# Performance work log

Hardware: AMD Instinct MI355X
Metric: run time of the kernel (lower is better)

The kernel has to match this reference:

```python
import jax, jax.numpy as jnp
import numpy as np

# --- configuration (mirrors VFNet cfg) ---
B, NC = 1, 6                     # batch, surround cameras
C_IN, H_F, W_F = 64, 44, 80      # fused feature level (height//8, width//8)
XD, YD, ZD = 100, 100, 20        # voxel dims (x forward, inverse-depth spaced)
X0, X1 = 2.0, 51.5
Y0, Y1 = -25.0, 24.5
Z0, Z1 = -3.0, 2.7
DB, D_STR, D_END = 50, 2.0, 50.0 # projection depth bins (inverse-depth spaced)
VDIM, FOUT = 64, 256             # voxel_pre_dim, feat_out_dim
P = H_F * W_F
EPS = 1e-8


def _axes():
    ego_x = 1.0 / jnp.linspace(1.0 / X1, 1.0 / X0, XD)[::-1]  # ascending, nonuniform
    ego_y = jnp.linspace(Y0, Y1, YD)
    ego_z = jnp.linspace(Z0, Z1, ZD)
    return ego_x, ego_y, ego_z


def _voxel_pts():
    ex, ey, ez = _axes()
    gz, gy, gx = jnp.meshgrid(ez, ey, ex, indexing='ij')      # [Z,Y,X]
    pts = jnp.stack([gx, gy, gz], 0).reshape(3, -1)
    return jnp.concatenate([pts, jnp.ones((1, pts.shape[1]), pts.dtype)], 0)  # [4,N]


def _bilinear2d(img, u, v):
    C, H, W = img.shape
    u0, v0 = jnp.floor(u), jnp.floor(v)
    du, dv = u - u0, v - v0
    u0i = jnp.clip(u0.astype(jnp.int32), 0, W - 1); u1i = jnp.clip(u0i + 1, 0, W - 1)
    v0i = jnp.clip(v0.astype(jnp.int32), 0, H - 1); v1i = jnp.clip(v0i + 1, 0, H - 1)
    g = lambda vi, ui: img[:, vi, ui]
    return (g(v0i, u0i) * (1 - du) * (1 - dv) + g(v0i, u1i) * du * (1 - dv)
            + g(v1i, u0i) * (1 - du) * dv + g(v1i, u1i) * du * dv)


def _nonuniform_index(axis, q):
    # searchsorted + in-bin lerp: metric coord -> continuous index on nonuniform axis
    qc = jnp.clip(q, axis[0], axis[-1] - 1e-6)
    k = jnp.clip(jnp.searchsorted(axis, qc, side='left') - 1, 0, axis.shape[0] - 2)
    t = (qc - axis[k]) / (axis[k + 1] - axis[k] + 1e-12)
    return k.astype(qc.dtype) + t


def _trilinear(vol, xi, yi, zi):
    Cc, Zz, Yy, Xx = vol.shape
    def sp(i, n):
        i0 = jnp.floor(i); t = i - i0
        a = jnp.clip(i0.astype(jnp.int32), 0, n - 1)
        return a, jnp.clip(a + 1, 0, n - 1), t
    x0, x1, tx = sp(xi, Xx); y0, y1, ty = sp(yi, Yy); z0, z1, tz = sp(zi, Zz)
    g = lambda z, y, x: vol[:, z, y, x]
    c0 = (g(z0, y0, x0) * (1 - tx) + g(z0, y0, x1) * tx) * (1 - ty) + (g(z0, y1, x0) * (1 - tx) + g(z0, y1, x1) * tx) * ty
    c1 = (g(z1, y0, x0) * (1 - tx) + g(z1, y0, x1) * tx) * (1 - ty) + (g(z1, y1, x0) * (1 - tx) + g(z1, y1, x1) * tx) * ty
    return c0 * (1 - tz) + c1 * tz


def _conv2d(x, w, b):
    y = jax.lax.conv_general_dilated(x, w, (1, 1), 'SAME', dimension_numbers=('NCHW', 'OIHW', 'NCHW'))
    return y + b[None, :, None, None]


def _conv3d(x, w, b):
    y = jax.lax.conv_general_dilated(x, w, (1, 1, 1), 'SAME', dimension_numbers=('NCDHW', 'OIDHW', 'NCDHW'))
    return y + b[None, :, None, None, None]


def _forward(feats, masks, K, ext, w_ov, b_ov, w_no, b_no, w_fu, b_fu, w_r1, b_r1, w_r2, b_r2):
    ex, ey, ez = _axes()
    vpts = _voxel_pts()                                        # [4,N]
    fm = jnp.concatenate([feats[0], masks[0]], axis=1)         # [NC, C+1, H, W]
    ext_inv = jnp.linalg.inv(ext)

    # --- backproject surround-view features into the nonuniform voxel grid ---
    def per_cam(img, Kc, Ei):
        pix = Kc @ (Ei @ vpts)
        z = pix[2]
        u = pix[0] / (z + EPS); v = pix[1] / (z + EPS)
        valid = (z > EPS) & (u >= 0) & (u <= W_F - 1) & (v >= 0) & (v <= H_F - 1)
        return _bilinear2d(img, u, v) * valid, valid.astype(img.dtype)

    s, valid = jax.vmap(per_cam)(fm, K, ext_inv)               # [NC,C+1,N], [NC,N]
    count = valid.sum(0)
    cat = jnp.concatenate([s[:3].sum(0), s[3:].sum(0)], axis=0)  # [2*(C+1),N]
    ov = jax.nn.elu(w_ov @ cat + b_ov[:, None]) * (count == 2)
    no = jax.nn.elu(w_no @ s.sum(0) + b_no[:, None]) * (count == 1)
    vf = (ov + no).reshape(VDIM, ZD, YD, XD)                   # [64,Z,Y,X]

    # --- nonuniform-x -> uniform-x remap (searchsorted + lerp) + conv3d fusion ---
    xi_axis = _nonuniform_index(ex, jnp.linspace(X0, X1, XD))
    ZI, YI, XI = jnp.meshgrid(jnp.arange(ZD, dtype=vf.dtype), jnp.arange(YD, dtype=vf.dtype), xi_axis, indexing='ij')
    vf_remap = _trilinear(vf, XI, YI, ZI)
    vol = jax.nn.elu(_conv3d(jnp.concatenate([vf, vf_remap], 0)[None], w_fu, b_fu))[0]  # [64,Z,Y,X]

    # --- project fused voxel features into each camera frustum over inv-depth bins ---
    uu, vv = jnp.meshgrid(jnp.arange(W_F), jnp.arange(H_F), indexing='xy')
    pix_grid = jnp.stack([uu.reshape(-1).astype(feats.dtype), vv.reshape(-1).astype(feats.dtype), jnp.ones((P,), feats.dtype)], 0)  # [3,P]
    dbins = 1.0 / jnp.linspace(1.0 / D_END, 1.0 / D_STR, DB)[::-1]  # ascending, inv-depth spaced
    K3inv = jnp.linalg.inv(K[:, :3, :3])

    def per_cam_proj(Ki, Ec):
        dirs = Ki @ pix_grid                                   # [3,P]
        pc = dirs[:, None, :] * dbins[None, :, None]           # [3,D,P]
        pc = jnp.concatenate([pc, jnp.ones((1, DB, P), pc.dtype)], 0)
        pw = (Ec @ pc.reshape(4, -1)).reshape(4, DB, P)        # ego-frame points
        wx, wy, wz = pw[0], pw[1], pw[2]
        xi = _nonuniform_index(ex, wx)
        yi = (wy - Y0) / (Y1 - Y0) * (YD - 1)
        zi = (wz - Z0) / (Z1 - Z0) * (ZD - 1)
        inb = (wx >= X0) & (wx <= X1) & (yi >= 0) & (yi <= YD - 1) & (zi >= 0) & (zi <= ZD - 1)
        samp = _trilinear(vol, xi, yi, zi) * inb               # [64,D,P]
        return samp.reshape(VDIM * DB, H_F, W_F)

    proj = jax.vmap(per_cam_proj)(K3inv, ext)                  # [NC, 64*D, H, W]
    h = jax.nn.elu(_conv2d(proj, w_r1, b_r1))
    return jax.nn.elu(_conv2d(h, w_r2, b_r2))                  # [NC, 256, H, W]


def setup_inputs() -> dict:
    key = jax.random.key(0)
    ks = jax.random.split(key, 8)
    feats = jax.random.normal(ks[0], (B, NC, C_IN, H_F, W_F), jnp.float32)
    masks = jnp.ones((B, NC, 1, H_F, W_F), jnp.float32)
    Kn = np.eye(4, dtype=np.float32)
    Kn[0, 0] = Kn[1, 1] = 40.0; Kn[0, 2] = 40.0; Kn[1, 2] = 22.0  # ~90deg hfov at 80px
    K = np.tile(Kn, (NC, 1, 1))
    ext = np.zeros((NC, 4, 4), dtype=np.float32)
    for i in range(NC):
        th = 2 * np.pi * i / NC
        c, s0 = np.cos(th), np.sin(th)
        R = np.array([[s0, 0, c], [-c, 0, s0], [0, -1, 0]], dtype=np.float32)  # cam(right,down,fwd)->ego
        ext[i, :3, :3] = R
        ext[i, :3, 3] = np.array([c, s0, 0.8], dtype=np.float32)
        ext[i, 3, 3] = 1.0
    w_ov = jax.random.normal(ks[1], (VDIM, 2 * (C_IN + 1)), jnp.float32) / np.sqrt(2 * (C_IN + 1)).astype(np.float32)
    w_no = jax.random.normal(ks[2], (VDIM, C_IN + 1), jnp.float32) / np.sqrt(C_IN + 1).astype(np.float32)
    w_fu = jax.random.normal(ks[3], (VDIM, 2 * VDIM, 3, 3, 3), jnp.float32) / np.sqrt(2 * VDIM * 27).astype(np.float32)
    w_r1 = jax.random.normal(ks[4], (FOUT, VDIM * DB, 3, 3), jnp.float32) / np.sqrt(VDIM * DB * 9).astype(np.float32)
    w_r2 = jax.random.normal(ks[5], (FOUT, FOUT, 3, 3), jnp.float32) / np.sqrt(FOUT * 9).astype(np.float32)
    z = lambda n: jnp.zeros((n,), jnp.float32)
    return {"feats": feats, "masks": masks, "K": jnp.asarray(K), "ext": jnp.asarray(ext),
            "w_ov": w_ov, "b_ov": z(VDIM), "w_no": w_no, "b_no": z(VDIM),
            "w_fu": w_fu, "b_fu": z(VDIM), "w_r1": w_r1, "b_r1": z(FOUT),
            "w_r2": w_r2, "b_r2": z(FOUT)}


def reference(feats, masks, K, ext, w_ov, b_ov, w_no, b_no, w_fu, b_fu, w_r1, b_r1, w_r2, b_r2):
    return _forward(feats, masks, K, ext, w_ov, b_ov, w_no, b_no, w_fu, b_fu, w_r1, b_r1, w_r2, b_r2)
```

## Files before the change

### kernel.cpp

```cpp
#include <hip/hip_runtime.h>
#include <math.h>

#define NCAM 6
#define CIN  64
#define HF   44
#define WF   80
#define PP   (HF*WF)
#define XD   100
#define YD   100
#define ZD   20
#define NVOX (XD*YD*ZD)
#define DBN  50
#define VDIM 64
#define FOUT 256
#define EPSF 1e-8f

typedef _Float16 f16x4 __attribute__((ext_vector_type(4)));
typedef _Float16 f16x8 __attribute__((ext_vector_type(8)));
typedef float    f32x4 __attribute__((ext_vector_type(4)));

#define OFF_KE    0
#define OFF_K3I   96
#define OFF_XI    160
#define OFF_DBIN  260
#define OFF_WOVT  320
#define OFF_WNOT  8640
#define B_VOL     51200UL
#define B_WT1     51200UL
#define B_H       14796800UL
#define B_VIN     25651200UL
#define B_PROJ    25651200UL
#define B_WT2     25651200UL
#define B_WT3     76851200UL

__device__ __forceinline__ float eluf(float x) { return x > 0.f ? x : expm1f(x); }

#define AX_A    (1.0f/51.5f)
#define AX_STEP ((0.5f - 1.0f/51.5f)/99.0f)

__device__ __forceinline__ void inv3x3(const float m[9], float o[9]) {
    float a00 = m[4]*m[8] - m[5]*m[7];
    float a10 = m[5]*m[6] - m[3]*m[8];
    float a20 = m[3]*m[7] - m[4]*m[6];
    float det = m[0]*a00 + m[1]*a10 + m[2]*a20;
    float id = 1.0f/det;
    o[0] = a00*id;
    o[1] = (m[2]*m[7] - m[1]*m[8])*id;
    o[2] = (m[1]*m[5] - m[2]*m[4])*id;
    o[3] = a10*id;
    o[4] = (m[0]*m[8] - m[2]*m[6])*id;
    o[5] = (m[2]*m[3] - m[0]*m[5])*id;
    o[6] = a20*id;
    o[7] = (m[1]*m[6] - m[0]*m[7])*id;
    o[8] = (m[0]*m[4] - m[1]*m[3])*id;
}

__global__ __launch_bounds__(256) void setup_kernel(const float* K, const float* ext,
                                                    const float* w_ov, const float* w_no,
                                                    float* ws) {
    int t = threadIdx.x;
    if (t < NCAM) {
        const float* E = ext + t*16;
        float R[9] = {E[0],E[1],E[2], E[4],E[5],E[6], E[8],E[9],E[10]};
        float Ri[9];
        inv3x3(R, Ri);
        float tx=E[3], ty=E[7], tz=E[11];
        float bx = -(Ri[0]*tx + Ri[1]*ty + Ri[2]*tz);
        float by = -(Ri[3]*tx + Ri[4]*ty + Ri[5]*tz);
        float bz = -(Ri[6]*tx + Ri[7]*ty + Ri[8]*tz);
        float Ei[16] = {Ri[0],Ri[1],Ri[2],bx, Ri[3],Ri[4],Ri[5],by, Ri[6],Ri[7],Ri[8],bz, 0,0,0,1};
        const float* Km = K + t*16;
        float* KE = ws + OFF_KE + t*16;
        for (int r=0;r<4;r++)
            for (int c=0;c<4;c++) {
                float s=0.f;
                for (int k=0;k<4;k++) s += Km[r*4+k]*Ei[k*4+c];
                KE[r*4+c]=s;
            }
        float Kr[9] = {Km[0],Km[1],Km[2], Km[4],Km[5],Km[6], Km[8],Km[9],Km[10]};
        float Ki[9];
        inv3x3(Kr, Ki);
        float* KI = ws + OFF_K3I + t*9;
        for (int i=0;i<9;i++) KI[i]=Ki[i];
    }
    if (t >= 64 && t < 64+XD) {
        int x = t-64;
        float ex0 = 1.0f/(AX_A + 99.0f*AX_STEP);
        float exN = 1.0f/AX_A;
        float q = 2.0f + (float)x * (49.5f/99.0f);
        float qc = fminf(fmaxf(q, ex0), exN - 1e-6f);
        float f = 99.0f - (1.0f/qc - AX_A)/AX_STEP;
        int k = min(max((int)floorf(f),0),98);
        float exk  = 1.0f/(AX_A + (float)(99-k)*AX_STEP);
        float exk1 = 1.0f/(AX_A + (float)(98-k)*AX_STEP);
        ws[OFF_XI + x] = (float)k + (qc - exk)/(exk1 - exk + 1e-12f);
    }
    if (t >= 192 && t < 192+DBN) {
        int d = t-192;
        float sa = 1.0f/50.0f;
        float ss = (0.5f - sa)/49.0f;
        ws[OFF_DBIN + d] = 1.0f/(sa + (float)(49-d)*ss);
    }
    for (int i = t; i < 130*64; i += 256) {
        int k = i >> 6, c = i & 63;
        ws[OFF_WOVT + i] = w_ov[c*130 + k];
    }
    for (int i = t; i < 65*64; i += 256) {
        int k = i >> 6, c = i & 63;
        ws[OFF_WNOT + i] = w_no[c*65 + k];
    }
}

__global__ __launch_bounds__(256) void tw1_kernel(const float* w, _Float16* o) {
    int idx = blockIdx.x*256 + threadIdx.x;
    int cp  = idx % 3200;
    int oc  = (idx/3200) & 255;
    int tap = idx/(3200*256);
    int d = cp >> 6, v = cp & 63;
    o[idx] = (_Float16)w[((size_t)oc*3200 + v*50 + d)*9 + tap];
}
__global__ __launch_bounds__(256) void tw2_kernel(const float* w, _Float16* o) {
    int idx = blockIdx.x*256 + threadIdx.x;
    int ic  = idx & 255;
    int oc  = (idx >> 8) & 255;
    int tap = idx >> 16;
    o[idx] = (_Float16)w[((size_t)oc*256 + ic)*9 + tap];
}
__global__ __launch_bounds__(256) void tw3_kernel(const float* w, _Float16* o) {
    int idx = blockIdx.x*256 + threadIdx.x;
    int ci  = idx & 127;
    int oc  = (idx >> 7) & 63;
    int tap = idx >> 13;
    o[idx] = (_Float16)w[((size_t)oc*128 + ci)*27 + tap];
}

__global__ __launch_bounds__(256) void backproject_kernel(const float* feats, const float* masks,
                                                          const float* ws,
                                                          const float* b_ov, const float* b_no,
                                                          _Float16* vin) {
    int wave = threadIdx.x >> 6;
    int lane = threadIdx.x & 63;
    int n = blockIdx.x*4 + wave;
    int x = n % XD;
    int y = (n / XD) % YD;
    int z = n / (XD*YD);
    float gx = 1.0f/(AX_A + (float)(99-x)*AX_STEP);
    float gy = -25.0f + (float)y * (49.5f/99.0f);
    float gz = -3.0f  + (float)z * (5.7f/19.0f);

    float sA = 0.f, sB = 0.f, sA64 = 0.f, sB64 = 0.f;
    int cnt = 0;
    for (int cam = 0; cam < NCAM; ++cam) {
        const float* KE = ws + OFF_KE + cam*16;
        float px = KE[0]*gx + KE[1]*gy + KE[2]*gz + KE[3];
        float py = KE[4]*gx + KE[5]*gy + KE[6]*gz + KE[7];
        float pz = KE[8]*gx + KE[9]*gy + KE[10]*gz + KE[11];
        float inv = 1.0f/(pz + EPSF);
        float u = px*inv, v = py*inv;
        bool valid = (pz > EPSF) && (u >= 0.f) && (u <= 79.f) && (v >= 0.f) && (v <= 43.f);
        if (valid) {
            cnt++;
            float u0 = floorf(u), v0 = floorf(v);
            float du = u-u0, dv = v-v0;
            int u0i = min(max((int)u0,0),WF-1), u1i = min(u0i+1,WF-1);
            int v0i = min(max((int)v0,0),HF-1), v1i = min(v0i+1,HF-1);
            float w00=(1.f-du)*(1.f-dv), w01=du*(1.f-dv), w10=(1.f-du)*dv, w11=du*dv;
            int i00=v0i*WF+u0i, i01=v0i*WF+u1i, i10=v1i*WF+u0i, i11=v1i*WF+u1i;
            const float* img = feats + (cam*CIN + lane)*PP;
            float val = w00*img[i00] + w01*img[i01] + w10*img[i10] + w11*img[i11];
            const float* mg = masks + cam*PP;
            float mv = w00*mg[i00] + w01*mg[i01] + w10*mg[i10] + w11*mg[i11];
            if (cam < 3) { sA += val; sA64 += mv; }
            else         { sB += val; sB64 += mv; }
        }
    }
    float out = 0.f;
    if (cnt == 2) {
        const float* wT = ws + OFF_WOVT;
        float acc = b_ov[lane];
        for (int k = 0; k < 64; ++k) {
            float ca = __shfl(sA, k, 64);
            float cb = __shfl(sB, k, 64);
            acc += wT[k*64 + lane]*ca + wT[(65+k)*64 + lane]*cb;
        }
        acc += wT[64*64 + lane]*sA64 + wT[129*64 + lane]*sB64;
        out = eluf(acc);
    } else if (cnt == 1) {
        const float* wT = ws + OFF_WNOT;
        float s = sA + sB, s64 = sA64 + sB64;
        float acc = b_no[lane];
        for (int k = 0; k < 64; ++k) {
            float ca = __shfl(s, k, 64);
            acc += wT[k*64 + lane]*ca;
        }
        acc += wT[64*64 + lane]*s64;
        out = eluf(acc);
    }
    vin[(size_t)n*128 + lane] = (_Float16)out;
}

__global__ __launch_bounds__(256) void remap_kernel(const float* ws, _Float16* vin) {
    int wave = threadIdx.x >> 6, lane = threadIdx.x & 63;
    int n = blockIdx.x*4 + wave;
    int x = n % XD;
    float xi = ws[OFF_XI + x];
    float fx = floorf(xi);
    float t = xi - fx;
    int x0 = min(max((int)fx,0),XD-1);
    int x1 = min(x0+1, XD-1);
    size_t rowb = (size_t)(n - x)*128;
    float r = (float)vin[rowb + (size_t)x0*128 + lane]*(1.f-t)
            + (float)vin[rowb + (size_t)x1*128 + lane]*t;
    vin[(size_t)n*128 + 64 + lane] = (_Float16)r;
}

__global__ __launch_bounds__(256,2) void conv3d_mfma_kernel(const _Float16* __restrict__ vin,
                                                            const _Float16* __restrict__ wT,
                                                            const float* __restrict__ bias,
                                                            _Float16* __restrict__ vol) {
    __shared__ __align__(16) _Float16 Bs[9*104*36];
    int tid = threadIdx.x, lane = tid & 63, wave = tid >> 6;
    int ln = lane & 15, kq = lane >> 4;
    int y = blockIdx.x % 100, z = blockIdx.x / 100;
    int nt0 = wave*2;
    int ntn = (wave == 3) ? 1 : 2;
    f32x4 zero4 = {0.f,0.f,0.f,0.f};
    f32x4 acc[4][2];
    for (int i=0;i<4;i++) for (int t=0;t<2;t++) acc[i][t] = zero4;

    for (int c0 = 0; c0 < 128; c0 += 32) {
        __syncthreads();
        for (int g = tid; g < 9*104*4; g += 256) {
            int ic8 = g & 3;
            int xe  = (g >> 2) % 104;
            int rid = g / (104*4);
            int xx = xe - 1, yy = y + rid%3 - 1, zz = z + rid/3 - 1;
            f16x8 val = {0,0,0,0,0,0,0,0};
            if (xx >= 0 && xx < 100 && yy >= 0 && yy < 100 && zz >= 0 && zz < 20)
                val = *(const f16x8*)(vin + (size_t)((zz*100 + yy)*100 + xx)*128 + c0 + ic8*8);
            *(f16x8*)(&Bs[(rid*104 + xe)*36 + ic8*8]) = val;
        }
        __syncthreads();
        const _Float16* wp0 = wT + c0 + kq*8;
        f16x8 a0n = *(const f16x8*)(wp0 + (ln+ 0)*128);
        f16x8 a1n = *(const f16x8*)(wp0 + (ln+16)*128);
        f16x8 a2n = *(const f16x8*)(wp0 + (ln+32)*128);
        f16x8 a3n = *(const f16x8*)(wp0 + (ln+48)*128);
        for (int tap = 0; tap < 27; ++tap) {
            f16x8 a0 = a0n, a1 = a1n, a2 = a2n, a3 = a3n;
            if (tap < 26) {
                const _Float16* wp = wT + (size_t)(tap+1)*64*128 + c0 + kq*8;
                a0n = *(const f16x8*)(wp + (ln+ 0)*128);
                a1n = *(const f16x8*)(wp + (ln+16)*128);
                a2n = *(const f16x8*)(wp + (ln+32)*128);
                a3n = *(const f16x8*)(wp + (ln+48)*128);
            }
            int dx = tap % 3, rid = tap / 3;
            for (int t = 0; t < ntn; ++t) {
                int xe = min(16*(nt0+t) + ln + dx, 103);
                f16x8 b = *(const f16x8*)(&Bs[(rid*104 + xe)*36 + kq*8]);
                acc[0][t] = __builtin_amdgcn_mfma_f32_16x16x32_f16(a0, b, acc[0][t], 0,0,0);
                acc[1][t] = __builtin_amdgcn_mfma_f32_16x16x32_f16(a1, b, acc[1][t], 0,0,0);
                acc[2][t] = __builtin_amdgcn_mfma_f32_16x16x32_f16(a2, b, acc[2][t], 0,0,0);
                acc[3][t] = __builtin_amdgcn_mfma_f32_16x16x32_f16(a3, b, acc[3][t], 0,0,0);
            }
        }
    }
    for (int i = 0; i < 4; ++i) {
        int oc0 = i*16 + kq*4;
        f32x4 bv = *(const f32x4*)(bias + oc0);
        for (int t = 0; t < ntn; ++t) {
            int x = 16*(nt0+t) + ln;
            if (x < 100) {
                size_t n = (size_t)(z*100 + y)*100 + x;
                f16x4 s;
                s[0] = (_Float16)eluf(acc[i][t][0] + bv[0]);
                s[1] = (_Float16)eluf(acc[i][t][1] + bv[1]);
                s[2] = (_Float16)eluf(acc[i][t][2] + bv[2]);
                s[3] = (_Float16)eluf(acc[i][t][3] + bv[3]);
                *(f16x4*)(vol + n*64 + oc0) = s;
            }
        }
    }
}

__global__ __launch_bounds__(256) void project_kernel(const float* ws, const float* ext,
                                                      const _Float16* vol, _Float16* proj) {
    __shared__ unsigned s_off[256][8];
    __shared__ float    s_w[256][8];
    int tid = threadIdx.x;
    int item = blockIdx.x*256 + tid;
    int d = item % 50;
    int p = (item/50) % 3520;
    int cam = item / (50*3520);
    {
        float uu = (float)(p % WF), vv = (float)(p / WF);
        const float* KI = ws + OFF_K3I + cam*9;
        float dxr = KI[0]*uu + KI[1]*vv + KI[2];
        float dyr = KI[3]*uu + KI[4]*vv + KI[5];
        float dzr = KI[6]*uu + KI[7]*vv + KI[8];
        float dep = ws[OFF_DBIN + d];
        float cx = dxr*dep, cy = dyr*dep, cz = dzr*dep;
        const float* E = ext + cam*16;
        float wx = E[0]*cx + E[1]*cy + E[2]*cz  + E[3];
        float wy = E[4]*cx + E[5]*cy + E[6]*cz  + E[7];
        float wz = E[8]*cx + E[9]*cy + E[10]*cz + E[11];
        float ex0 = 1.0f/(AX_A + 99.0f*AX_STEP);
        float exN = 1.0f/AX_A;
        float qc = fminf(fmaxf(wx, ex0), exN - 1e-6f);
        float f = 99.0f - (1.0f/qc - AX_A)/AX_STEP;
        int k = min(max((int)floorf(f),0),98);
        float exk  = 1.0f/(AX_A + (float)(99-k)*AX_STEP);
        float exk1 = 1.0f/(AX_A + (float)(98-k)*AX_STEP);
        float xi = (float)k + (qc - exk)/(exk1 - exk + 1e-12f);
        float yi = (wy + 25.0f) * (99.0f/49.5f);
        float zi = (wz + 3.0f)  * (19.0f/5.7f);
        float scale = ((wx >= 2.0f) && (wx <= 51.5f) && (yi >= 0.f) && (yi <= 99.f)
                       && (zi >= 0.f) && (zi <= 19.f)) ? 1.f : 0.f;
        float fx = floorf(xi), fy = floorf(yi), fz = floorf(zi);
        float tx = xi-fx, ty = yi-fy, tz = zi-fz;
        int x0 = min(max((int)fx,0),XD-1), x1 = min(x0+1,XD-1);
        int y0 = min(max((int)fy,0),YD-1), y1 = min(y0+1,YD-1);
        int z0 = min(max((int)fz,0),ZD-1), z1 = min(z0+1,ZD-1);
        s_off[tid][0] = (unsigned)(((z0*YD+y0)*XD+x0)*64); s_w[tid][0] = (1.f-tx)*(1.f-ty)*(1.f-tz)*scale;
        s_off[tid][1] = (unsigned)(((z0*YD+y0)*XD+x1)*64); s_w[tid][1] = tx*(1.f-ty)*(1.f-tz)*scale;
        s_off[tid][2] = (unsigned)(((z0*YD+y1)*XD+x0)*64); s_w[tid][2] = (1.f-tx)*ty*(1.f-tz)*scale;
        s_off[tid][3] = (unsigned)(((z0*YD+y1)*XD+x1)*64); s_w[tid][3] = tx*ty*(1.f-tz)*scale;
        s_off[tid][4] = (unsigned)(((z1*YD+y0)*XD+x0)*64); s_w[tid][4] = (1.f-tx)*(1.f-ty)*tz*scale;
        s_off[tid][5] = (unsigned)(((z1*YD+y0)*XD+x1)*64); s_w[tid][5] = tx*(1.f-ty)*tz*scale;
        s_off[tid][6] = (unsigned)(((z1*YD+y1)*XD+x0)*64); s_w[tid][6] = (1.f-tx)*ty*tz*scale;
        s_off[tid][7] = (unsigned)(((z1*YD+y1)*XD+x1)*64); s_w[tid][7] = tx*ty*tz*scale;
    }
    __syncthreads();
    int wave = tid >> 6, lane = tid & 63;
    size_t outbase = (size_t)blockIdx.x*256 + wave*64;
    for (int j = 0; j < 64; ++j) {
        int it = wave*64 + j;
        float a = 0.f;
        #pragma unroll
        for (int c = 0; c < 8; ++c)
            a += s_w[it][c] * (float)vol[s_off[it][c] + lane];
        proj[(outbase + j)*64 + lane] = (_Float16)a;
    }
}

template<int ICN, bool OUT16>
__global__ __launch_bounds__(256,4) void conv2d_mfma_kernel(const _Float16* __restrict__ in,
                                                            const _Float16* __restrict__ wT,
                                                            const float* __restrict__ bias,
                                                            void* __restrict__ outp) {
    constexpr int NCH = ICN/32;
    constexpr int NSLOT = 6;
    __shared__ __align__(16) _Float16 Bs[4*82*36];
    int tid = threadIdx.x, lane = tid & 63, wave = tid >> 6;
    int wm = wave >> 1, wn = wave & 1;
    int ln = lane & 15, kq = lane >> 4;
    int bid = blockIdx.x;
    int ocq = bid & 3;
    int rest = bid >> 2;
    int cam = rest % 6;
    int h0 = (rest / 6)*2;
    int ocb = ocq*64 + wm*32;
    size_t campix0 = (size_t)cam*3520;
    f32x4 zero4 = {0.f,0.f,0.f,0.f};
    f32x4 acc[2][5];
    for (int i=0;i<2;i++) for (int t=0;t<5;t++) acc[i][t] = zero4;

    size_t soff[NSLOT];
    int    slds[NSLOT];
    bool   sok[NSLOT];
    #pragma unroll
    for (int i = 0; i < NSLOT; ++i) {
        int g = tid + i*256;
        if (g < 4*82*4) {
            int ic8 = g & 3;
            int we  = (g >> 2) % 82;
            int re  = g / (82*4);
            int h = h0 - 1 + re;
            int w = we - 1;
            sok[i]  = (h >= 0 && h < HF && w >= 0 && w < WF);
            soff[i] = (campix0 + h*80 + w)*(size_t)ICN + ic8*8;
            slds[i] = (re*82 + we)*36 + ic8*8;
        } else { sok[i] = false; soff[i] = 0; slds[i] = -1; }
    }

    f16x8 sreg[NSLOT];
    #pragma unroll
    for (int i = 0; i < NSLOT; ++i) {
        f16x8 v = {0,0,0,0,0,0,0,0};
        if (sok[i]) v = *(const f16x8*)(in + soff[i]);
        sreg[i] = v;
    }

    const _Float16* wbase0 = wT + (size_t)ocb*ICN + kq*8;
    for (int c = 0; c < NCH; ++c) {
        __syncthreads();
        #pragma unroll
        for (int i = 0; i < NSLOT; ++i)
            if (slds[i] >= 0) *(f16x8*)(&Bs[slds[i]]) = sreg[i];
        __syncthreads();
        if (c + 1 < NCH) {
            int c1 = (c+1)*32;
            #pragma unroll
            for (int i = 0; i < NSLOT; ++i) {
                f16x8 v = {0,0,0,0,0,0,0,0};
                if (sok[i]) v = *(const f16x8*)(in + soff[i] + c1);
                sreg[i] = v;
            }
        }
        const _Float16* wb = wbase0 + c*32;
        #pragma unroll
        for (int tg = 0; tg < 3; ++tg) {
            f16x8 A0[3], A1[3];
            #pragma unroll
            for (int j = 0; j < 3; ++j) {
                const _Float16* wp = wb + (size_t)(tg*3 + j)*256*ICN;
                A0[j] = *(const f16x8*)(wp + (size_t)(ln+ 0)*ICN);
                A1[j] = *(const f16x8*)(wp + (size_t)(ln+16)*ICN);
            }
            #pragma unroll
            for (int j = 0; j < 3; ++j) {
                int tap = tg*3 + j;
                int ky = tap/3, kx = tap%3;
                int rbase = (wn + ky)*82 + ln + kx;
                #pragma unroll
                for (int t = 0; t < 5; ++t) {
                    f16x8 b = *(const f16x8*)(&Bs[(rbase + 16*t)*36 + kq*8]);
                    acc[0][t] = __builtin_amdgcn_mfma_f32_16x16x32_f16(A0[j], b, acc[0][t], 0,0,0);
                    acc[1][t] = __builtin_amdgcn_mfma_f32_16x16x32_f16(A1[j], b, acc[1][t], 0,0,0);
                }
            }
        }
    }
    int pixrow = h0 + wn;
    for (int i = 0; i < 2; ++i) {
        int oc0 = ocb + i*16 + kq*4;
        f32x4 bv = *(const f32x4*)(bias + oc0);
        for (int t = 0; t < 5; ++t) {
            int pix = pixrow*80 + 16*t + ln;
            float v0 = eluf(acc[i][t][0] + bv[0]);
            float v1 = eluf(acc[i][t][1] + bv[1]);
            float v2 = eluf(acc[i][t][2] + bv[2]);
            float v3 = eluf(acc[i][t][3] + bv[3]);
            if (OUT16) {
                f16x4 s; s[0]=(_Float16)v0; s[1]=(_Float16)v1; s[2]=(_Float16)v2; s[3]=(_Float16)v3;
                *(f16x4*)((_Float16*)outp + (campix0 + pix)*256 + oc0) = s;
            } else {
                float* op = (float*)outp + ((size_t)(cam*256 + oc0))*PP + pix;
                op[0] = v0; op[PP] = v1; op[2*PP] = v2; op[3*PP] = v3;
            }
        }
    }
}

extern "C" void kernel_launch(void* const* d_in, const int* in_sizes, int n_in,
                              void* d_out, int out_size, void* d_ws, size_t ws_size,
                              hipStream_t stream) {
    const float* feats = (const float*)d_in[0];
    const float* masks = (const float*)d_in[1];
    const float* K     = (const float*)d_in[2];
    const float* ext   = (const float*)d_in[3];
    const float* w_ov  = (const float*)d_in[4];
    const float* b_ov  = (const float*)d_in[5];
    const float* w_no  = (const float*)d_in[6];
    const float* b_no  = (const float*)d_in[7];
    const float* w_fu  = (const float*)d_in[8];
    const float* b_fu  = (const float*)d_in[9];
    const float* w_r1  = (const float*)d_in[10];
    const float* b_r1  = (const float*)d_in[11];
    const float* w_r2  = (const float*)d_in[12];
    const float* b_r2  = (const float*)d_in[13];
    char* base = (char*)d_ws;
    float*    wsf  = (float*)base;
    _Float16* vol  = (_Float16*)(base + B_VOL);
    _Float16* wT1  = (_Float16*)(base + B_WT1);
    _Float16* h    = (_Float16*)(base + B_H);
    _Float16* vin  = (_Float16*)(base + B_VIN);
    _Float16* proj = (_Float16*)(base + B_PROJ);
    _Float16* wT2  = (_Float16*)(base + B_WT2);
    _Float16* wT3  = (_Float16*)(base + B_WT3);
    float* out = (float*)d_out;

    setup_kernel<<<1, 256, 0, stream>>>(K, ext, w_ov, w_no, wsf);
    tw3_kernel<<<(27*64*128)/256, 256, 0, stream>>>(w_fu, wT3);
    backproject_kernel<<<NVOX/4, 256, 0, stream>>>(feats, masks, wsf, b_ov, b_no, vin);
    remap_kernel<<<NVOX/4, 256, 0, stream>>>(wsf, vin);
    conv3d_mfma_kernel<<<ZD*YD, 256, 0, stream>>>(vin, wT3, b_fu, vol);
    project_kernel<<<(NCAM*PP*DBN)/256, 256, 0, stream>>>(wsf, ext, vol, proj);
    tw1_kernel<<<(9*256*3200)/256, 256, 0, stream>>>(w_r1, wT1);
    conv2d_mfma_kernel<3200, true><<<4*NCAM*22, 256, 0, stream>>>(proj, wT1, b_r1, h);
    tw2_kernel<<<(9*256*256)/256, 256, 0, stream>>>(w_r2, wT2);
    conv2d_mfma_kernel<256, false><<<4*NCAM*22, 256, 0, stream>>>(h, wT2, b_r2, out);
}
```

Baseline: 1.811 ms.

## Split conv2d reduction across waves with one output row per block

The 2D conv kernel now gives each block a single output row instead of two, which doubles the grid. The two wave groups that used to handle different rows now split the input-channel reduction, each taking half of a 64-channel chunk, and their partial sums are combined through LDS before the bias and ELU epilogue. The shared-memory tile uses an XOR swizzle in place of padding to avoid bank conflicts. The register prefetch of the next chunk is removed, so global loads are no longer overlapped with MFMA work, and each block has fewer chunk iterations. Halving rows per block also raises the weight-load traffic per output pixel.

```diff
diff --git a/kernel.cpp b/kernel.cpp
--- a/kernel.cpp
+++ b/kernel.cpp
@@ -349,17 +349,17 @@
                                                             const _Float16* __restrict__ wT,
                                                             const float* __restrict__ bias,
                                                             void* __restrict__ outp) {
-    constexpr int NCH = ICN/32;
-    constexpr int NSLOT = 6;
-    __shared__ __align__(16) _Float16 Bs[4*82*36];
+    constexpr int NCH = ICN/64;
+    constexpr int NG  = 3*82*8;
+    constexpr int NSLOT = (NG + 255)/256;
+    __shared__ __align__(16) _Float16 Bs[3*82*64];
     int tid = threadIdx.x, lane = tid & 63, wave = tid >> 6;
     int wm = wave >> 1, wn = wave & 1;
     int ln = lane & 15, kq = lane >> 4;
     int bid = blockIdx.x;
-    int ocq = bid & 3;
-    int rest = bid >> 2;
-    int cam = rest % 6;
-    int h0 = (rest / 6)*2;
+    int h0  = bid % 44;
+    int cam = (bid/44) % 6;
+    int ocq = bid / 264;
     int ocb = ocq*64 + wm*32;
     size_t campix0 = (size_t)cam*3520;
     f32x4 zero4 = {0.f,0.f,0.f,0.f};
@@ -372,43 +372,33 @@
     #pragma unroll
     for (int i = 0; i < NSLOT; ++i) {
         int g = tid + i*256;
-        if (g < 4*82*4) {
-            int ic8 = g & 3;
-            int we  = (g >> 2) % 82;
-            int re  = g / (82*4);
-            int h = h0 - 1 + re;
+        if (g < NG) {
+            int kg  = g & 7;
+            int we  = (g >> 3) % 82;
+            int rid = g / (82*8);
+            int h = h0 - 1 + rid;
             int w = we - 1;
-            sok[i]  = (h >= 0 && h < HF && w >= 0 && w < WF);
-            soff[i] = (campix0 + h*80 + w)*(size_t)ICN + ic8*8;
-            slds[i] = (re*82 + we)*36 + ic8*8;
+            sok[i]  = (g < NG) && (h >= 0 && h < HF && w >= 0 && w < WF);
+            soff[i] = (campix0 + h*80 + w)*(size_t)ICN + kg*8;
+            slds[i] = (rid*82 + we)*64 + ((kg ^ (we & 7))*8);
         } else { sok[i] = false; soff[i] = 0; slds[i] = -1; }
     }
 
-    f16x8 sreg[NSLOT];
-    #pragma unroll
-    for (int i = 0; i < NSLOT; ++i) {
-        f16x8 v = {0,0,0,0,0,0,0,0};
-        if (sok[i]) v = *(const f16x8*)(in + soff[i]);
-        sreg[i] = v;
-    }
-
-    const _Float16* wbase0 = wT + (size_t)ocb*ICN + kq*8;
+    const int kh = wn*32 + kq*8;
+    const _Float16* wbase0 = wT + (size_t)ocb*ICN + kh;
     for (int c = 0; c < NCH; ++c) {
+        int c0 = c*64;
         __syncthreads();
         #pragma unroll
-        for (int i = 0; i < NSLOT; ++i)
-            if (slds[i] >= 0) *(f16x8*)(&Bs[slds[i]]) = sreg[i];
+        for (int i = 0; i < NSLOT; ++i) {
+            if (slds[i] >= 0) {
+                f16x8 v = {0,0,0,0,0,0,0,0};
+                if (sok[i]) v = *(const f16x8*)(in + soff[i] + c0);
+                *(f16x8*)(&Bs[slds[i]]) = v;
+            }
+        }
         __syncthreads();
-        if (c + 1 < NCH) {
-            int c1 = (c+1)*32;
-            #pragma unroll
-            for (int i = 0; i < NSLOT; ++i) {
-                f16x8 v = {0,0,0,0,0,0,0,0};
-                if (sok[i]) v = *(const f16x8*)(in + soff[i] + c1);
-                sreg[i] = v;
-            }
-        }
-        const _Float16* wb = wbase0 + c*32;
+        const _Float16* wb = wbase0 + c0;
         #pragma unroll
         for (int tg = 0; tg < 3; ++tg) {
             f16x8 A0[3], A1[3];
@@ -422,32 +412,50 @@
             for (int j = 0; j < 3; ++j) {
                 int tap = tg*3 + j;
                 int ky = tap/3, kx = tap%3;
-                int rbase = (wn + ky)*82 + ln + kx;
+                int swz = ((wn*4 + kq) ^ ((ln + kx) & 7))*8;
+                int rbase = (ky*82 + ln + kx)*64 + swz;
                 #pragma unroll
                 for (int t = 0; t < 5; ++t) {
-                    f16x8 b = *(const f16x8*)(&Bs[(rbase + 16*t)*36 + kq*8]);
+                    f16x8 b = *(const f16x8*)(&Bs[rbase + t*1024]);
                     acc[0][t] = __builtin_amdgcn_mfma_f32_16x16x32_f16(A0[j], b, acc[0][t], 0,0,0);
                     acc[1][t] = __builtin_amdgcn_mfma_f32_16x16x32_f16(A1[j], b, acc[1][t], 0,0,0);
                 }
             }
         }
     }
-    int pixrow = h0 + wn;
-    for (int i = 0; i < 2; ++i) {
-        int oc0 = ocb + i*16 + kq*4;
-        f32x4 bv = *(const f32x4*)(bias + oc0);
-        for (int t = 0; t < 5; ++t) {
-            int pix = pixrow*80 + 16*t + ln;
-            float v0 = eluf(acc[i][t][0] + bv[0]);
-            float v1 = eluf(acc[i][t][1] + bv[1]);
-            float v2 = eluf(acc[i][t][2] + bv[2]);
-            float v3 = eluf(acc[i][t][3] + bv[3]);
-            if (OUT16) {
-                f16x4 s; s[0]=(_Float16)v0; s[1]=(_Float16)v1; s[2]=(_Float16)v2; s[3]=(_Float16)v3;
-                *(f16x4*)((_Float16*)outp + (campix0 + pix)*256 + oc0) = s;
-            } else {
-                float* op = (float*)outp + ((size_t)(cam*256 + oc0))*PP + pix;
-                op[0] = v0; op[PP] = v1; op[2*PP] = v2; op[3*PP] = v3;
+
+    __syncthreads();
+    float* mbuf = (float*)Bs;
+    if (wn == 1) {
+        float* mb = mbuf + (wm*64 + lane)*40;
+        #pragma unroll
+        for (int i = 0; i < 2; ++i)
+            #pragma unroll
+            for (int t = 0; t < 5; ++t)
+                *(f32x4*)(mb + (i*5+t)*4) = acc[i][t];
+    }
+    __syncthreads();
+    if (wn == 0) {
+        const float* mb = mbuf + (wm*64 + lane)*40;
+        #pragma unroll
+        for (int i = 0; i < 2; ++i) {
+            int oc0 = ocb + i*16 + kq*4;
+            f32x4 bv = *(const f32x4*)(bias + oc0);
+            #pragma unroll
+            for (int t = 0; t < 5; ++t) {
+                f32x4 p = *(const f32x4*)(mb + (i*5+t)*4);
+                int pix = h0*80 + 16*t + ln;
+                float v0 = eluf(acc[i][t][0] + p[0] + bv[0]);
+                float v1 = eluf(acc[i][t][1] + p[1] + bv[1]);
+                float v2 = eluf(acc[i][t][2] + p[2] + bv[2]);
+                float v3 = eluf(acc[i][t][3] + p[3] + bv[3]);
+                if (OUT16) {
+                    f16x4 s; s[0]=(_Float16)v0; s[1]=(_Float16)v1; s[2]=(_Float16)v2; s[3]=(_Float16)v3;
+                    *(f16x4*)((_Float16*)outp + (campix0 + pix)*256 + oc0) = s;
+                } else {
+                    float* op = (float*)outp + ((size_t)(cam*256 + oc0))*PP + pix;
+                    op[0] = v0; op[PP] = v1; op[2*PP] = v2; op[3*PP] = v3;
+                }
             }
         }
     }
@@ -488,7 +496,7 @@
     conv3d_mfma_kernel<<<ZD*YD, 256, 0, stream>>>(vin, wT3, b_fu, vol);
     project_kernel<<<(NCAM*PP*DBN)/256, 256, 0, stream>>>(wsf, ext, vol, proj);
     tw1_kernel<<<(9*256*3200)/256, 256, 0, stream>>>(w_r1, wT1);
-    conv2d_mfma_kernel<3200, true><<<4*NCAM*22, 256, 0, stream>>>(proj, wT1, b_r1, h);
+    conv2d_mfma_kernel<3200, true><<<4*NCAM*44, 256, 0, stream>>>(proj, wT1, b_r1, h);
     tw2_kernel<<<(9*256*256)/256, 256, 0, stream>>>(w_r2, wT2);
-    conv2d_mfma_kernel<256, false><<<4*NCAM*22, 256, 0, stream>>>(h, wT2, b_r2, out);
-}
+    conv2d_mfma_kernel<256, false><<<4*NCAM*44, 256, 0, stream>>>(h, wT2, b_r2, out);
+}
```

New measurement: 1.855 ms. +2.4%, slower.
